# Kernel optimization log

Hardware: AMD Instinct MI355X
Metric: run time of the kernel (lower is better)

The kernel has to match this reference:

```python
import jax, jax.numpy as jnp
import numpy as np

DIM, H, DH = 1024, 16, 64
SCALE = 1.0 / np.sqrt(DH)


def setup_inputs() -> dict:
    key = jax.random.key(0)
    ks = jax.random.split(key, 16)
    B, S = 2, 2048
    glorot = jax.nn.initializers.glorot_uniform()
    def qkv(k):
        return glorot(k, (DIM, H, DH), jnp.float32)
    inp = {
        "x": jax.random.normal(ks[0], (B, S, DIM), jnp.float32),
        "layer_idx": 3,
        "lambda_param": jnp.full((1,), 0.8, jnp.float32),
    }
    for i, br in enumerate(["1", "2"]):
        base = 1 + i * 4
        inp[f"Wq{br}"] = qkv(ks[base])
        inp[f"Wk{br}"] = qkv(ks[base + 1])
        inp[f"Wv{br}"] = qkv(ks[base + 2])
        inp[f"Wo{br}"] = glorot(ks[base + 3], (H, DH, DIM), jnp.float32).reshape(H, DH, DIM)
        inp[f"bq{br}"] = jnp.zeros((H, DH), jnp.float32)
        inp[f"bk{br}"] = jnp.zeros((H, DH), jnp.float32)
        inp[f"bv{br}"] = jnp.zeros((H, DH), jnp.float32)
        inp[f"bo{br}"] = jnp.zeros((DIM,), jnp.float32)
    inp["Wp"] = glorot(ks[9], (DIM, DIM), jnp.float32)
    inp["bp"] = jnp.zeros((DIM,), jnp.float32)
    return inp


def _mha(x, Wq, bq, Wk, bk, Wv, bv, Wo, bo):
    # x: [B,S,D]; per-head projections as in keras.layers.MultiHeadAttention
    q = jnp.einsum("bsd,dhk->bshk", x, Wq) + bq   # [B,S,H,Dh]
    k = jnp.einsum("bsd,dhk->bshk", x, Wk) + bk
    v = jnp.einsum("bsd,dhk->bshk", x, Wv) + bv
    scores = jnp.einsum("bqhd,bkhd->bhqk", q, k) * SCALE  # [B,H,S,S]
    attn = jax.nn.softmax(scores, axis=-1)
    o = jnp.einsum("bhqk,bkhd->bqhd", attn, v)            # [B,S,H,Dh]
    return jnp.einsum("bqhd,hdo->bqo", o, Wo) + bo        # [B,S,D]


def _get_lambda(lambda_param, layer_idx):
    lf = jnp.asarray(layer_idx, jnp.float32)
    exp_term = jnp.exp(-0.3 * jnp.maximum(lf - 1.0, 0.0))
    init = 0.8 - 0.6 * exp_term
    return jnp.clip(init * lambda_param[0], 0.1, 0.9)


def reference(x, layer_idx, lambda_param,
              Wq1, bq1, Wk1, bk1, Wv1, bv1, Wo1, bo1,
              Wq2, bq2, Wk2, bk2, Wv2, bv2, Wo2, bo2,
              Wp, bp):
    a1 = _mha(x, Wq1, bq1, Wk1, bk1, Wv1, bv1, Wo1, bo1)
    a2 = _mha(x, Wq2, bq2, Wk2, bk2, Wv2, bv2, Wo2, bo2)
    lam = _get_lambda(lambda_param, layer_idx)
    diff = a1 - lam * a2
    return diff @ Wp + bp  # dropout is identity at inference
```

## Files before the change

### kernel.cpp

```cpp
#include <hip/hip_runtime.h>
#include <math.h>

typedef unsigned short u16;
typedef __attribute__((ext_vector_type(8))) short bf16x8;
typedef __attribute__((ext_vector_type(4))) float f32x4;
typedef __attribute__((ext_vector_type(4))) unsigned short u16x4;
typedef __attribute__((ext_vector_type(8))) unsigned short u16x8;

constexpr int Sq = 2048, Dm = 1024, Hh = 16, DH = 64;
constexpr int NT = 4096;
constexpr float SEXP = 0.125f * 1.44269504f;

__device__ __forceinline__ u16 f2bf(float f) {
    unsigned u = __float_as_uint(f);
    return (u16)((u + 0x7FFF + ((u >> 16) & 1)) >> 16);
}

__device__ __forceinline__ void async16(u16* lds, const u16* g) {
    __builtin_amdgcn_global_load_lds(
        (const __attribute__((address_space(1))) unsigned int*)g,
        (__attribute__((address_space(3))) unsigned int*)lds, 16, 0, 0);
}

__device__ __forceinline__ float lam_of(const int* lidx, const float* lamp) {
    float lf = (float)lidx[0];
    float init = 0.8f - 0.6f * __expf(-0.3f * fmaxf(lf - 1.0f, 0.0f));
    return fminf(fmaxf(init * lamp[0], 0.1f), 0.9f);
}

__device__ __forceinline__ void gemm_tile_128(
    const u16* __restrict__ A, const u16* __restrict__ Bt, int K,
    int aRow0, int bCol0, u16* As, u16* Bs, f32x4 acc[4][4])
{
    const int tid = threadIdx.x;
    const int w = tid >> 6, lane = tid & 63;
    const int ln = lane & 15, quad = lane >> 4;
    const int wm = (w >> 1) * 64, wn = (w & 1) * 64;
    const int l3 = lane & 7, lr8 = lane >> 3;

    for (int kt = 0; kt < K; kt += 64) {
        __syncthreads();
        #pragma unroll
        for (int c0 = 0; c0 < 4; ++c0) {
            int c = w * 4 + c0;
            int lr = c * 8 + lr8;
            int sc = l3 ^ (lr & 7);
            async16(As + c * 512, A + (size_t)(aRow0 + lr) * K + kt + sc * 8);
            async16(Bs + c * 512, Bt + (size_t)(bCol0 + lr) * K + kt + sc * 8);
        }
        __syncthreads();
        #pragma unroll
        for (int kc = 0; kc < 2; ++kc) {
            bf16x8 af[4], bfr[4];
            #pragma unroll
            for (int mt = 0; mt < 4; ++mt)
                af[mt] = *(const bf16x8*)(As + (wm + mt * 16 + ln) * 64 +
                                          (((kc * 4 + quad) ^ (ln & 7)) * 8));
            #pragma unroll
            for (int nt = 0; nt < 4; ++nt)
                bfr[nt] = *(const bf16x8*)(Bs + (wn + nt * 16 + ln) * 64 +
                                           (((kc * 4 + quad) ^ (ln & 7)) * 8));
            #pragma unroll
            for (int mt = 0; mt < 4; ++mt)
                #pragma unroll
                for (int nt = 0; nt < 4; ++nt)
                    acc[mt][nt] = __builtin_amdgcn_mfma_f32_16x16x32_bf16(
                        af[mt], bfr[nt], acc[mt][nt], 0, 0, 0);
        }
    }
}

__device__ __forceinline__ void gemm_tile_64(
    const u16* __restrict__ A, const u16* __restrict__ Bt, int K,
    int aRow0, int bCol0, u16* As, u16* Bs, f32x4 acc[2][4])
{
    const int tid = threadIdx.x;
    const int w = tid >> 6, lane = tid & 63;
    const int ln = lane & 15, quad = lane >> 4;
    const int wm = (w >> 1) * 32, wn = (w & 1) * 64;
    const int l3 = lane & 7, lr8 = lane >> 3;

    for (int kt = 0; kt < K; kt += 64) {
        __syncthreads();
        #pragma unroll
        for (int c0 = 0; c0 < 2; ++c0) {
            int c = w * 2 + c0;
            int lr = c * 8 + lr8;
            int sc = l3 ^ (lr & 7);
            async16(As + c * 512, A + (size_t)(aRow0 + lr) * K + kt + sc * 8);
        }
        #pragma unroll
        for (int c0 = 0; c0 < 4; ++c0) {
            int c = w * 4 + c0;
            int lr = c * 8 + lr8;
            int sc = l3 ^ (lr & 7);
            async16(Bs + c * 512, Bt + (size_t)(bCol0 + lr) * K + kt + sc * 8);
        }
        __syncthreads();
        #pragma unroll
        for (int kc = 0; kc < 2; ++kc) {
            bf16x8 af[2], bfr[4];
            #pragma unroll
            for (int mt = 0; mt < 2; ++mt)
                af[mt] = *(const bf16x8*)(As + (wm + mt * 16 + ln) * 64 +
                                          (((kc * 4 + quad) ^ (ln & 7)) * 8));
            #pragma unroll
            for (int nt = 0; nt < 4; ++nt)
                bfr[nt] = *(const bf16x8*)(Bs + (wn + nt * 16 + ln) * 64 +
                                           (((kc * 4 + quad) ^ (ln & 7)) * 8));
            #pragma unroll
            for (int mt = 0; mt < 2; ++mt)
                #pragma unroll
                for (int nt = 0; nt < 4; ++nt)
                    acc[mt][nt] = __builtin_amdgcn_mfma_f32_16x16x32_bf16(
                        af[mt], bfr[nt], acc[mt][nt], 0, 0, 0);
        }
    }
}

__global__ __launch_bounds__(256)
void convert_x(const float* __restrict__ x, u16* __restrict__ xb)
{
    int i = (blockIdx.x * 256 + threadIdx.x) * 4;
    float4 v = *(const float4*)(x + i);
    u16x4 o;
    o.x = f2bf(v.x); o.y = f2bf(v.y); o.z = f2bf(v.z); o.w = f2bf(v.w);
    *(u16x4*)(xb + i) = o;
}

struct TcP { const float* src[9]; u16* dst[9]; int ld[9]; int coff[9]; };

__global__ __launch_bounds__(256)
void wconv(TcP p, const int* __restrict__ lidx, const float* __restrict__ lamp)
{
    __shared__ float t[64][65];
    const int z = blockIdx.z;
    const float scale = (z == 7) ? -lam_of(lidx, lamp) : 1.0f;
    const float* __restrict__ src = p.src[z];
    u16* __restrict__ dst = p.dst[z];
    const int kb = blockIdx.y * 64, nb = blockIdx.x * 64;
    const int tid = threadIdx.x;
    {
        int r = tid >> 2, cs = (tid & 3) * 16;
        #pragma unroll
        for (int j4 = 0; j4 < 16; j4 += 4) {
            float4 v = *(const float4*)&src[(size_t)(kb + r) * 1024 + nb + cs + j4];
            t[r][cs + j4 + 0] = v.x; t[r][cs + j4 + 1] = v.y;
            t[r][cs + j4 + 2] = v.z; t[r][cs + j4 + 3] = v.w;
        }
    }
    __syncthreads();
    {
        int n = tid >> 2, ks = (tid & 3) * 16;
        u16x8 a, b;
        #pragma unroll
        for (int j = 0; j < 8; ++j) a[j] = f2bf(scale * t[ks + j][n]);
        #pragma unroll
        for (int j = 0; j < 8; ++j) b[j] = f2bf(scale * t[ks + 8 + j][n]);
        u16* o = &dst[(size_t)(nb + n) * p.ld[z] + p.coff[z] + kb + ks];
        *(u16x8*)o = a;
        *(u16x8*)(o + 8) = b;
    }
}

struct QkvP { const u16* Wt[6]; const float* bias[6]; u16* out[6]; };

__global__ __launch_bounds__(256, 3)
void qkv_mfma(const u16* __restrict__ xb, QkvP p)
{
    __shared__ u16 As[128 * 64], Bs[128 * 64];
    const int z = blockIdx.z;
    const int type = (z < 3) ? z : z - 3;
    const int aRow0 = blockIdx.y * 128, nCol0 = blockIdx.x * 128;
    f32x4 acc[4][4] = {};
    gemm_tile_128(xb, p.Wt[z], 1024, aRow0, nCol0, As, Bs, acc);

    const float* __restrict__ bias = p.bias[z];
    u16* __restrict__ out = p.out[z];
    const int tid = threadIdx.x, w = tid >> 6, lane = tid & 63;
    const int ln = lane & 15, quad = lane >> 4;
    const int wm = (w >> 1) * 64, wn = (w & 1) * 64;
    #pragma unroll
    for (int mt = 0; mt < 4; ++mt) {
        #pragma unroll
        for (int nt = 0; nt < 4; ++nt) {
            int gn = nCol0 + wn + nt * 16 + ln;
            int h = gn >> 6, dh = gn & 63;
            float bv = bias[gn];
            #pragma unroll
            for (int r = 0; r < 4; ++r) {
                int gm = aRow0 + wm + mt * 16 + quad * 4 + r;
                int b = gm >> 11, s = gm & (Sq - 1);
                size_t bh = (size_t)(b * Hh + h);
                float fv = acc[mt][nt][r] + bv;
                size_t idx;
                u16 val;
                if (type == 0) {
                    val = f2bf(fv * SEXP);
                    idx = bh * 131072 + (size_t)s * 64 + dh;
                } else if (type == 1) {
                    val = f2bf(fv);
                    idx = bh * 131072 + (size_t)(s >> 5) * 2048 +
                          (size_t)((dh >> 5) * 2 + ((s >> 4) & 1)) * 512 +
                          (size_t)(((dh >> 3) & 3) * 16 + (s & 15)) * 8 + (dh & 7);
                } else {
                    val = f2bf(fv);
                    int kidx = ((s & 15) * 2) + ((s >> 4) & 1);
                    idx = bh * 131072 + (size_t)(s >> 5) * 2048 +
                          (size_t)(dh >> 4) * 512 +
                          (size_t)((kidx >> 3) * 16 + (dh & 15)) * 8 + (kidx & 7);
                }
                out[idx] = val;
            }
        }
    }
}

__global__ __launch_bounds__(256, 4)
void attn_mfma(const u16* __restrict__ q1, const u16* __restrict__ kf1,
               const u16* __restrict__ vf1,
               const u16* __restrict__ q2, const u16* __restrict__ kf2,
               const u16* __restrict__ vf2, u16* __restrict__ ocat)
{
    __shared__ __align__(16) char smem[10240];

    const int bh = blockIdx.x, qblk = blockIdx.y, br = blockIdx.z;
    const u16* __restrict__ q  = br ? q2  : q1;
    const u16* __restrict__ kf = br ? kf2 : kf1;
    const u16* __restrict__ vf = br ? vf2 : vf1;

    const int tid = threadIdx.x, w = tid >> 6, lane = tid & 63;
    const int ln = lane & 15, quad = lane >> 4;
    char* Pbase = smem + w * 2560;

    const u16* qbase = q + (size_t)bh * 131072 +
                       (size_t)(qblk * 128 + w * 32) * 64;
    bf16x8 qf[2][2];
    #pragma unroll
    for (int mt = 0; mt < 2; ++mt)
        #pragma unroll
        for (int kc = 0; kc < 2; ++kc)
            qf[mt][kc] = *(const bf16x8*)(qbase + (mt * 16 + ln) * 64 +
                                          kc * 32 + quad * 8);

    bf16x8 ones;
    #pragma unroll
    for (int j = 0; j < 8; ++j) ones[j] = (short)0x3F80;

    f32x4 oacc[2][4] = {};
    f32x4 lacc[2] = {};

    const u16* kbase = kf + (size_t)bh * 131072 + lane * 8;
    const u16* vbase = vf + (size_t)bh * 131072 + lane * 8;

    for (int kt = 0; kt < 64; ++kt) {
        const u16* kp = kbase + (size_t)kt * 2048;
        const u16* vp = vbase + (size_t)kt * 2048;

        bf16x8 kfr[2][2];
        #pragma unroll
        for (int kc = 0; kc < 2; ++kc)
            #pragma unroll
            for (int nt = 0; nt < 2; ++nt)
                kfr[nt][kc] = *(const bf16x8*)(kp + (kc * 2 + nt) * 512);

        f32x4 sacc[2][2] = {};
        #pragma unroll
        for (int kc = 0; kc < 2; ++kc)
            #pragma unroll
            for (int mt = 0; mt < 2; ++mt)
                #pragma unroll
                for (int nt = 0; nt < 2; ++nt)
                    sacc[mt][nt] = __builtin_amdgcn_mfma_f32_16x16x32_bf16(
                        qf[mt][kc], kfr[nt][kc], sacc[mt][nt], 0, 0, 0);

        #pragma unroll
        for (int mt = 0; mt < 2; ++mt) {
            #pragma unroll
            for (int r = 0; r < 4; ++r) {
                float p0 = exp2f(sacc[mt][0][r]);
                float p1 = exp2f(sacc[mt][1][r]);
                unsigned a  = __float_as_uint(p0) + 0x8000u;
                unsigned b2 = __float_as_uint(p1) + 0x8000u;
                unsigned pk = __builtin_amdgcn_perm(b2, a, 0x07060302);
                int row = mt * 16 + quad * 4 + r;
                *(unsigned*)(Pbase + row * 80 + (((ln >> 2) ^ r) << 4) +
                             ((ln & 3) << 2)) = pk;
            }
        }

        bf16x8 vfr[4];
        #pragma unroll
        for (int dt = 0; dt < 4; ++dt)
            vfr[dt] = *(const bf16x8*)(vp + dt * 512);

        #pragma unroll
        for (int mt = 0; mt < 2; ++mt) {
            bf16x8 pf = *(const bf16x8*)(Pbase + (mt * 16 + ln) * 80 +
                                         ((quad ^ (ln & 3)) << 4));
            lacc[mt] = __builtin_amdgcn_mfma_f32_16x16x32_bf16(
                pf, ones, lacc[mt], 0, 0, 0);
            #pragma unroll
            for (int dt = 0; dt < 4; ++dt)
                oacc[mt][dt] = __builtin_amdgcn_mfma_f32_16x16x32_bf16(
                    pf, vfr[dt], oacc[mt][dt], 0, 0, 0);
        }

        __builtin_amdgcn_s_barrier();
    }

    const int b = bh >> 4, h = bh & 15;
    #pragma unroll
    for (int mt = 0; mt < 2; ++mt) {
        #pragma unroll
        for (int r = 0; r < 4; ++r) {
            float inv = 1.0f / lacc[mt][r];
            int s = qblk * 128 + w * 32 + mt * 16 + quad * 4 + r;
            size_t rowb = (size_t)(b * Sq + s) * 2048 + br * 1024 + h * 64;
            #pragma unroll
            for (int dt = 0; dt < 4; ++dt)
                ocat[rowb + dt * 16 + ln] = f2bf(oacc[mt][dt][r] * inv);
        }
    }
}

__global__ __launch_bounds__(256, 4)
void combine_mfma(const u16* __restrict__ ocat, const u16* __restrict__ Wcmb,
                  const float* __restrict__ bo1, const float* __restrict__ bo2,
                  const int* __restrict__ lidx, const float* __restrict__ lamp,
                  u16* __restrict__ adiff)
{
    __shared__ u16 As[64 * 64], Bs[128 * 64];
    const int aRow0 = blockIdx.y * 64, nCol0 = blockIdx.x * 128;
    f32x4 acc[2][4] = {};
    gemm_tile_64(ocat, Wcmb, 2048, aRow0, nCol0, As, Bs, acc);

    const float lam = lam_of(lidx, lamp);
    const int tid = threadIdx.x, w = tid >> 6, lane = tid & 63;
    const int ln = lane & 15, quad = lane >> 4;
    const int wm = (w >> 1) * 32, wn = (w & 1) * 64;
    #pragma unroll
    for (int mt = 0; mt < 2; ++mt) {
        #pragma unroll
        for (int nt = 0; nt < 4; ++nt) {
            int gn = nCol0 + wn + nt * 16 + ln;
            float bv = bo1[gn] - lam * bo2[gn];
            #pragma unroll
            for (int r = 0; r < 4; ++r) {
                int gm = aRow0 + wm + mt * 16 + quad * 4 + r;
                adiff[(size_t)gm * 1024 + gn] = f2bf(acc[mt][nt][r] + bv);
            }
        }
    }
}

__global__ __launch_bounds__(256, 4)
void final_mfma(const u16* __restrict__ adiff, const u16* __restrict__ Wpt,
                const float* __restrict__ bp, float* __restrict__ outb)
{
    __shared__ u16 As[64 * 64], Bs[128 * 64];
    const int aRow0 = blockIdx.y * 64, nCol0 = blockIdx.x * 128;
    f32x4 acc[2][4] = {};
    gemm_tile_64(adiff, Wpt, 1024, aRow0, nCol0, As, Bs, acc);

    const int tid = threadIdx.x, w = tid >> 6, lane = tid & 63;
    const int ln = lane & 15, quad = lane >> 4;
    const int wm = (w >> 1) * 32, wn = (w & 1) * 64;
    #pragma unroll
    for (int mt = 0; mt < 2; ++mt) {
        #pragma unroll
        for (int nt = 0; nt < 4; ++nt) {
            int gn = nCol0 + wn + nt * 16 + ln;
            float bv = bp[gn];
            #pragma unroll
            for (int r = 0; r < 4; ++r) {
                int gm = aRow0 + wm + mt * 16 + quad * 4 + r;
                outb[(size_t)gm * 1024 + gn] = acc[mt][nt][r] + bv;
            }
        }
    }
}

extern "C" void kernel_launch(void* const* d_in, const int* in_sizes, int n_in,
                              void* d_out, int out_size, void* d_ws, size_t ws_size,
                              hipStream_t stream)
{
    const float* x    = (const float*)d_in[0];
    const int*   lidx = (const int*)  d_in[1];
    const float* lamp = (const float*)d_in[2];
    const float* Wq1  = (const float*)d_in[3];
    const float* Wk1  = (const float*)d_in[4];
    const float* Wv1  = (const float*)d_in[5];
    const float* Wo1  = (const float*)d_in[6];
    const float* bq1  = (const float*)d_in[7];
    const float* bk1  = (const float*)d_in[8];
    const float* bv1  = (const float*)d_in[9];
    const float* bo1  = (const float*)d_in[10];
    const float* Wq2  = (const float*)d_in[11];
    const float* Wk2  = (const float*)d_in[12];
    const float* Wv2  = (const float*)d_in[13];
    const float* Wo2  = (const float*)d_in[14];
    const float* bq2  = (const float*)d_in[15];
    const float* bk2  = (const float*)d_in[16];
    const float* bv2  = (const float*)d_in[17];
    const float* bo2  = (const float*)d_in[18];
    const float* Wp   = (const float*)d_in[19];
    const float* bp   = (const float*)d_in[20];

    char* wsb = (char*)d_ws;
    const size_t MB = 1 << 20;
    u16* xb   = (u16*)(wsb + 0 * MB);
    u16* Wt0  = (u16*)(wsb + 8 * MB);
    u16* Wcmb = (u16*)(wsb + 20 * MB);
    u16* Wpt  = (u16*)(wsb + 24 * MB);
    u16* qb1  = (u16*)(wsb + 26 * MB);
    u16* kb1  = (u16*)(wsb + 34 * MB);
    u16* vb1  = (u16*)(wsb + 42 * MB);
    u16* qb2  = (u16*)(wsb + 50 * MB);
    u16* kb2  = (u16*)(wsb + 58 * MB);
    u16* vb2  = (u16*)(wsb + 66 * MB);
    u16* ocat = (u16*)(wsb + 74 * MB);
    u16* adif = (u16*)(wsb + 90 * MB);

    convert_x<<<dim3(NT * Dm / 1024), dim3(256), 0, stream>>>(x, xb);

    TcP tp;
    const float* wsrc[9] = {Wq1, Wk1, Wv1, Wq2, Wk2, Wv2, Wo1, Wo2, Wp};
    for (int i = 0; i < 9; ++i) tp.src[i] = wsrc[i];
    for (int i = 0; i < 6; ++i) { tp.dst[i] = Wt0 + (size_t)i * 1024 * 1024; tp.ld[i] = 1024; tp.coff[i] = 0; }
    tp.dst[6] = Wcmb; tp.ld[6] = 2048; tp.coff[6] = 0;
    tp.dst[7] = Wcmb; tp.ld[7] = 2048; tp.coff[7] = 1024;
    tp.dst[8] = Wpt;  tp.ld[8] = 1024; tp.coff[8] = 0;
    wconv<<<dim3(16, 16, 9), dim3(256), 0, stream>>>(tp, lidx, lamp);

    QkvP qp;
    qp.Wt[0] = Wt0 + 0 * 1048576; qp.bias[0] = bq1; qp.out[0] = qb1;
    qp.Wt[1] = Wt0 + 1 * 1048576; qp.bias[1] = bk1; qp.out[1] = kb1;
    qp.Wt[2] = Wt0 + 2 * 1048576; qp.bias[2] = bv1; qp.out[2] = vb1;
    qp.Wt[3] = Wt0 + 3 * 1048576; qp.bias[3] = bq2; qp.out[3] = qb2;
    qp.Wt[4] = Wt0 + 4 * 1048576; qp.bias[4] = bk2; qp.out[4] = kb2;
    qp.Wt[5] = Wt0 + 5 * 1048576; qp.bias[5] = bv2; qp.out[5] = vb2;
    qkv_mfma<<<dim3(8, 32, 6), dim3(256), 0, stream>>>(xb, qp);

    attn_mfma<<<dim3(32, 16, 2), dim3(256), 0, stream>>>(
        qb1, kb1, vb1, qb2, kb2, vb2, ocat);

    combine_mfma<<<dim3(8, 64), dim3(256), 0, stream>>>(
        ocat, Wcmb, bo1, bo2, lidx, lamp, adif);

    final_mfma<<<dim3(8, 64), dim3(256), 0, stream>>>(
        adif, Wpt, bp, (float*)d_out);
}
```

Baseline: 352.8 us.

## Fold output projections into a precomputed combined weight and streamline attention loop

Uses associativity to precompute Wfull = [Wo1; -lam*Wo2] @ Wp and a combined bias once per call. This replaces the two token-level GEMMs (combine then final) with one 4096x2048x1024 GEMM plus a small 2049x1024x1024 weight GEMM. It removes the adiff intermediate and one large GEMM pass. The attention loop is also unrolled by two tiles per barrier, starts the first score MFMA from a zero constant, and uses the raw hardware exp2 builtin. The risks are extra bf16 rounding of the fused weight and loss of range checks in exp2.

```diff
diff --git a/kernel.cpp b/kernel.cpp
--- a/kernel.cpp
+++ b/kernel.cpp
@@ -10,6 +10,12 @@
 constexpr int Sq = 2048, Dm = 1024, Hh = 16, DH = 64;
 constexpr int NT = 4096;
 constexpr float SEXP = 0.125f * 1.44269504f;
+
+#if __has_builtin(__builtin_amdgcn_exp2f)
+#define EXP2(x) __builtin_amdgcn_exp2f(x)
+#else
+#define EXP2(x) exp2f(x)
+#endif
 
 __device__ __forceinline__ u16 f2bf(float f) {
     unsigned u = __float_as_uint(f);
@@ -128,14 +134,13 @@
     *(u16x4*)(xb + i) = o;
 }
 
-struct TcP { const float* src[9]; u16* dst[9]; int ld[9]; int coff[9]; };
+struct TcP { const float* src[7]; u16* dst[7]; };
 
 __global__ __launch_bounds__(256)
-void wconv(TcP p, const int* __restrict__ lidx, const float* __restrict__ lamp)
+void wconv(TcP p)
 {
     __shared__ float t[64][65];
     const int z = blockIdx.z;
-    const float scale = (z == 7) ? -lam_of(lidx, lamp) : 1.0f;
     const float* __restrict__ src = p.src[z];
     u16* __restrict__ dst = p.dst[z];
     const int kb = blockIdx.y * 64, nb = blockIdx.x * 64;
@@ -154,12 +159,68 @@
         int n = tid >> 2, ks = (tid & 3) * 16;
         u16x8 a, b;
         #pragma unroll
-        for (int j = 0; j < 8; ++j) a[j] = f2bf(scale * t[ks + j][n]);
-        #pragma unroll
-        for (int j = 0; j < 8; ++j) b[j] = f2bf(scale * t[ks + 8 + j][n]);
-        u16* o = &dst[(size_t)(nb + n) * p.ld[z] + p.coff[z] + kb + ks];
+        for (int j = 0; j < 8; ++j) a[j] = f2bf(t[ks + j][n]);
+        #pragma unroll
+        for (int j = 0; j < 8; ++j) b[j] = f2bf(t[ks + 8 + j][n]);
+        u16* o = &dst[(size_t)(nb + n) * 1024 + kb + ks];
         *(u16x8*)o = a;
         *(u16x8*)(o + 8) = b;
+    }
+}
+
+__global__ __launch_bounds__(256)
+void woconv(const float* __restrict__ Wo1, const float* __restrict__ Wo2,
+            const float* __restrict__ bo1, const float* __restrict__ bo2,
+            const int* __restrict__ lidx, const float* __restrict__ lamp,
+            u16* __restrict__ Acat)
+{
+    const float lam = lam_of(lidx, lamp);
+    int i = (blockIdx.x * 256 + threadIdx.x) * 4;
+    float4 v;
+    if (i < 1048576) {
+        v = *(const float4*)(Wo1 + i);
+    } else if (i < 2097152) {
+        v = *(const float4*)(Wo2 + (i - 1048576));
+        v.x *= -lam; v.y *= -lam; v.z *= -lam; v.w *= -lam;
+    } else {
+        int c = i - 2097152;
+        float4 a = *(const float4*)(bo1 + c);
+        float4 b = *(const float4*)(bo2 + c);
+        v.x = a.x - lam * b.x; v.y = a.y - lam * b.y;
+        v.z = a.z - lam * b.z; v.w = a.w - lam * b.w;
+    }
+    u16x4 o;
+    o.x = f2bf(v.x); o.y = f2bf(v.y); o.z = f2bf(v.z); o.w = f2bf(v.w);
+    *(u16x4*)(Acat + i) = o;
+}
+
+__global__ __launch_bounds__(256, 4)
+void wfull_mfma(const u16* __restrict__ Acat, const u16* __restrict__ Wpt,
+                const float* __restrict__ bp, u16* __restrict__ Wfull_bt,
+                float* __restrict__ bfull)
+{
+    __shared__ u16 As[64 * 64], Bs[128 * 64];
+    const int aRow0 = blockIdx.y * 64, nCol0 = blockIdx.x * 128;
+    f32x4 acc[2][4] = {};
+    gemm_tile_64(Acat, Wpt, 1024, aRow0, nCol0, As, Bs, acc);
+
+    const int tid = threadIdx.x, w = tid >> 6, lane = tid & 63;
+    const int ln = lane & 15, quad = lane >> 4;
+    const int wm = (w >> 1) * 32, wn = (w & 1) * 64;
+    #pragma unroll
+    for (int mt = 0; mt < 2; ++mt) {
+        #pragma unroll
+        for (int nt = 0; nt < 4; ++nt) {
+            int gn = nCol0 + wn + nt * 16 + ln;
+            #pragma unroll
+            for (int r = 0; r < 4; ++r) {
+                int gm = aRow0 + wm + mt * 16 + quad * 4 + r;
+                if (gm < 2048)
+                    Wfull_bt[(size_t)gn * 2048 + gm] = f2bf(acc[mt][nt][r]);
+                else if (gm == 2048)
+                    bfull[gn] = acc[mt][nt][r] + bp[gn];
+            }
+        }
     }
 }
 
@@ -246,6 +307,7 @@
     bf16x8 ones;
     #pragma unroll
     for (int j = 0; j < 8; ++j) ones[j] = (short)0x3F80;
+    const f32x4 zero4 = {0.f, 0.f, 0.f, 0.f};
 
     f32x4 oacc[2][4] = {};
     f32x4 lacc[2] = {};
@@ -253,59 +315,66 @@
     const u16* kbase = kf + (size_t)bh * 131072 + lane * 8;
     const u16* vbase = vf + (size_t)bh * 131072 + lane * 8;
 
-    for (int kt = 0; kt < 64; ++kt) {
-        const u16* kp = kbase + (size_t)kt * 2048;
-        const u16* vp = vbase + (size_t)kt * 2048;
-
-        bf16x8 kfr[2][2];
-        #pragma unroll
-        for (int kc = 0; kc < 2; ++kc)
-            #pragma unroll
-            for (int nt = 0; nt < 2; ++nt)
-                kfr[nt][kc] = *(const bf16x8*)(kp + (kc * 2 + nt) * 512);
-
-        f32x4 sacc[2][2] = {};
-        #pragma unroll
-        for (int kc = 0; kc < 2; ++kc)
+    for (int it = 0; it < 32; ++it) {
+        #pragma unroll
+        for (int u = 0; u < 2; ++u) {
+            const int kt = it * 2 + u;
+            const u16* kp = kbase + (size_t)kt * 2048;
+            const u16* vp = vbase + (size_t)kt * 2048;
+
+            bf16x8 kfr[2][2];
+            #pragma unroll
+            for (int kc = 0; kc < 2; ++kc)
+                #pragma unroll
+                for (int nt = 0; nt < 2; ++nt)
+                    kfr[nt][kc] = *(const bf16x8*)(kp + (kc * 2 + nt) * 512);
+
+            f32x4 sacc[2][2];
             #pragma unroll
             for (int mt = 0; mt < 2; ++mt)
                 #pragma unroll
                 for (int nt = 0; nt < 2; ++nt)
                     sacc[mt][nt] = __builtin_amdgcn_mfma_f32_16x16x32_bf16(
-                        qf[mt][kc], kfr[nt][kc], sacc[mt][nt], 0, 0, 0);
-
-        #pragma unroll
-        for (int mt = 0; mt < 2; ++mt) {
-            #pragma unroll
-            for (int r = 0; r < 4; ++r) {
-                float p0 = exp2f(sacc[mt][0][r]);
-                float p1 = exp2f(sacc[mt][1][r]);
-                unsigned a  = __float_as_uint(p0) + 0x8000u;
-                unsigned b2 = __float_as_uint(p1) + 0x8000u;
-                unsigned pk = __builtin_amdgcn_perm(b2, a, 0x07060302);
-                int row = mt * 16 + quad * 4 + r;
-                *(unsigned*)(Pbase + row * 80 + (((ln >> 2) ^ r) << 4) +
-                             ((ln & 3) << 2)) = pk;
+                        qf[mt][0], kfr[nt][0], zero4, 0, 0, 0);
+            #pragma unroll
+            for (int mt = 0; mt < 2; ++mt)
+                #pragma unroll
+                for (int nt = 0; nt < 2; ++nt)
+                    sacc[mt][nt] = __builtin_amdgcn_mfma_f32_16x16x32_bf16(
+                        qf[mt][1], kfr[nt][1], sacc[mt][nt], 0, 0, 0);
+
+            #pragma unroll
+            for (int mt = 0; mt < 2; ++mt) {
+                #pragma unroll
+                for (int r = 0; r < 4; ++r) {
+                    float p0 = EXP2(sacc[mt][0][r]);
+                    float p1 = EXP2(sacc[mt][1][r]);
+                    unsigned a  = __float_as_uint(p0) + 0x8000u;
+                    unsigned b2 = __float_as_uint(p1) + 0x8000u;
+                    unsigned pk = __builtin_amdgcn_perm(b2, a, 0x07060302);
+                    int row = mt * 16 + quad * 4 + r;
+                    *(unsigned*)(Pbase + row * 80 + (((ln >> 2) ^ r) << 4) +
+                                 ((ln & 3) << 2)) = pk;
+                }
             }
-        }
-
-        bf16x8 vfr[4];
-        #pragma unroll
-        for (int dt = 0; dt < 4; ++dt)
-            vfr[dt] = *(const bf16x8*)(vp + dt * 512);
-
-        #pragma unroll
-        for (int mt = 0; mt < 2; ++mt) {
-            bf16x8 pf = *(const bf16x8*)(Pbase + (mt * 16 + ln) * 80 +
-                                         ((quad ^ (ln & 3)) << 4));
-            lacc[mt] = __builtin_amdgcn_mfma_f32_16x16x32_bf16(
-                pf, ones, lacc[mt], 0, 0, 0);
+
+            bf16x8 vfr[4];
             #pragma unroll
             for (int dt = 0; dt < 4; ++dt)
-                oacc[mt][dt] = __builtin_amdgcn_mfma_f32_16x16x32_bf16(
-                    pf, vfr[dt], oacc[mt][dt], 0, 0, 0);
-        }
-
+                vfr[dt] = *(const bf16x8*)(vp + dt * 512);
+
+            #pragma unroll
+            for (int mt = 0; mt < 2; ++mt) {
+                bf16x8 pf = *(const bf16x8*)(Pbase + (mt * 16 + ln) * 80 +
+                                             ((quad ^ (ln & 3)) << 4));
+                lacc[mt] = __builtin_amdgcn_mfma_f32_16x16x32_bf16(
+                    pf, ones, lacc[mt], 0, 0, 0);
+                #pragma unroll
+                for (int dt = 0; dt < 4; ++dt)
+                    oacc[mt][dt] = __builtin_amdgcn_mfma_f32_16x16x32_bf16(
+                        pf, vfr[dt], oacc[mt][dt], 0, 0, 0);
+            }
+        }
         __builtin_amdgcn_s_barrier();
     }
 
@@ -325,17 +394,14 @@
 }
 
 __global__ __launch_bounds__(256, 4)
-void combine_mfma(const u16* __restrict__ ocat, const u16* __restrict__ Wcmb,
-                  const float* __restrict__ bo1, const float* __restrict__ bo2,
-                  const int* __restrict__ lidx, const float* __restrict__ lamp,
-                  u16* __restrict__ adiff)
+void out_mfma(const u16* __restrict__ ocat, const u16* __restrict__ Wfull_bt,
+              const float* __restrict__ bfull, float* __restrict__ outb)
 {
     __shared__ u16 As[64 * 64], Bs[128 * 64];
     const int aRow0 = blockIdx.y * 64, nCol0 = blockIdx.x * 128;
     f32x4 acc[2][4] = {};
-    gemm_tile_64(ocat, Wcmb, 2048, aRow0, nCol0, As, Bs, acc);
-
-    const float lam = lam_of(lidx, lamp);
+    gemm_tile_64(ocat, Wfull_bt, 2048, aRow0, nCol0, As, Bs, acc);
+
     const int tid = threadIdx.x, w = tid >> 6, lane = tid & 63;
     const int ln = lane & 15, quad = lane >> 4;
     const int wm = (w >> 1) * 32, wn = (w & 1) * 64;
@@ -344,34 +410,7 @@
         #pragma unroll
         for (int nt = 0; nt < 4; ++nt) {
             int gn = nCol0 + wn + nt * 16 + ln;
-            float bv = bo1[gn] - lam * bo2[gn];
-            #pragma unroll
-            for (int r = 0; r < 4; ++r) {
-                int gm = aRow0 + wm + mt * 16 + quad * 4 + r;
-                adiff[(size_t)gm * 1024 + gn] = f2bf(acc[mt][nt][r] + bv);
-            }
-        }
-    }
-}
-
-__global__ __launch_bounds__(256, 4)
-void final_mfma(const u16* __restrict__ adiff, const u16* __restrict__ Wpt,
-                const float* __restrict__ bp, float* __restrict__ outb)
-{
-    __shared__ u16 As[64 * 64], Bs[128 * 64];
-    const int aRow0 = blockIdx.y * 64, nCol0 = blockIdx.x * 128;
-    f32x4 acc[2][4] = {};
-    gemm_tile_64(adiff, Wpt, 1024, aRow0, nCol0, As, Bs, acc);
-
-    const int tid = threadIdx.x, w = tid >> 6, lane = tid & 63;
-    const int ln = lane & 15, quad = lane >> 4;
-    const int wm = (w >> 1) * 32, wn = (w & 1) * 64;
-    #pragma unroll
-    for (int mt = 0; mt < 2; ++mt) {
-        #pragma unroll
-        for (int nt = 0; nt < 4; ++nt) {
-            int gn = nCol0 + wn + nt * 16 + ln;
-            float bv = bp[gn];
+            float bv = bfull[gn];
             #pragma unroll
             for (int r = 0; r < 4; ++r) {
                 int gm = aRow0 + wm + mt * 16 + quad * 4 + r;
@@ -409,29 +448,34 @@
 
     char* wsb = (char*)d_ws;
     const size_t MB = 1 << 20;
-    u16* xb   = (u16*)(wsb + 0 * MB);
-    u16* Wt0  = (u16*)(wsb + 8 * MB);
-    u16* Wcmb = (u16*)(wsb + 20 * MB);
-    u16* Wpt  = (u16*)(wsb + 24 * MB);
-    u16* qb1  = (u16*)(wsb + 26 * MB);
-    u16* kb1  = (u16*)(wsb + 34 * MB);
-    u16* vb1  = (u16*)(wsb + 42 * MB);
-    u16* qb2  = (u16*)(wsb + 50 * MB);
-    u16* kb2  = (u16*)(wsb + 58 * MB);
-    u16* vb2  = (u16*)(wsb + 66 * MB);
-    u16* ocat = (u16*)(wsb + 74 * MB);
-    u16* adif = (u16*)(wsb + 90 * MB);
+    u16* xb    = (u16*)(wsb + 0 * MB);
+    u16* Wt0   = (u16*)(wsb + 8 * MB);
+    u16* Wpt   = (u16*)(wsb + 20 * MB);
+    u16* Acat  = (u16*)(wsb + 22 * MB);
+    u16* Wfull = (u16*)(wsb + 27 * MB);
+    float* bfull = (float*)(wsb + 31 * MB);
+    u16* qb1   = (u16*)(wsb + 32 * MB);
+    u16* kb1   = (u16*)(wsb + 40 * MB);
+    u16* vb1   = (u16*)(wsb + 48 * MB);
+    u16* qb2   = (u16*)(wsb + 56 * MB);
+    u16* kb2   = (u16*)(wsb + 64 * MB);
+    u16* vb2   = (u16*)(wsb + 72 * MB);
+    u16* ocat  = (u16*)(wsb + 80 * MB);
 
     convert_x<<<dim3(NT * Dm / 1024), dim3(256), 0, stream>>>(x, xb);
 
     TcP tp;
-    const float* wsrc[9] = {Wq1, Wk1, Wv1, Wq2, Wk2, Wv2, Wo1, Wo2, Wp};
-    for (int i = 0; i < 9; ++i) tp.src[i] = wsrc[i];
-    for (int i = 0; i < 6; ++i) { tp.dst[i] = Wt0 + (size_t)i * 1024 * 1024; tp.ld[i] = 1024; tp.coff[i] = 0; }
-    tp.dst[6] = Wcmb; tp.ld[6] = 2048; tp.coff[6] = 0;
-    tp.dst[7] = Wcmb; tp.ld[7] = 2048; tp.coff[7] = 1024;
-    tp.dst[8] = Wpt;  tp.ld[8] = 1024; tp.coff[8] = 0;
-    wconv<<<dim3(16, 16, 9), dim3(256), 0, stream>>>(tp, lidx, lamp);
+    const float* wsrc[7] = {Wq1, Wk1, Wv1, Wq2, Wk2, Wv2, Wp};
+    for (int i = 0; i < 7; ++i) tp.src[i] = wsrc[i];
+    for (int i = 0; i < 6; ++i) tp.dst[i] = Wt0 + (size_t)i * 1024 * 1024;
+    tp.dst[6] = Wpt;
+    wconv<<<dim3(16, 16, 7), dim3(256), 0, stream>>>(tp);
+
+    woconv<<<dim3(2049), dim3(256), 0, stream>>>(
+        Wo1, Wo2, bo1, bo2, lidx, lamp, Acat);
+
+    wfull_mfma<<<dim3(8, 33), dim3(256), 0, stream>>>(
+        Acat, Wpt, bp, Wfull, bfull);
 
     QkvP qp;
     qp.Wt[0] = Wt0 + 0 * 1048576; qp.bias[0] = bq1; qp.out[0] = qb1;
@@ -445,9 +489,6 @@
     attn_mfma<<<dim3(32, 16, 2), dim3(256), 0, stream>>>(
         qb1, kb1, vb1, qb2, kb2, vb2, ocat);
 
-    combine_mfma<<<dim3(8, 64), dim3(256), 0, stream>>>(
-        ocat, Wcmb, bo1, bo2, lidx, lamp, adif);
-
-    final_mfma<<<dim3(8, 64), dim3(256), 0, stream>>>(
-        adif, Wpt, bp, (float*)d_out);
-}
+    out_mfma<<<dim3(8, 64), dim3(256), 0, stream>>>(
+        ocat, Wfull, bfull, (float*)d_out);
+}
```

Result: faster. 333.2 us (-5.6%).
